# Kernel optimization log

Measured on AMD Instinct MI355X. Metric: run time of the kernel, lower is better.

Reference implementation:

```python
import jax, jax.numpy as jnp
import numpy as np

D_IN = 1024
D_OUT = 1024
B = 4
S = 2048


def setup_inputs() -> dict:
    key = jax.random.key(0)
    kx, kq, kk, kv = jax.random.split(key, 4)
    x = jax.random.normal(kx, (B, S, D_IN), dtype=jnp.float32)
    # Linear weights stored as [d_in, d_out] so projection is x @ W
    sc = 1.0 / np.sqrt(D_IN)
    Wq = jax.random.normal(kq, (D_IN, D_OUT), dtype=jnp.float32) * sc
    Wk = jax.random.normal(kk, (D_IN, D_OUT), dtype=jnp.float32) * sc
    Wv = jax.random.normal(kv, (D_IN, D_OUT), dtype=jnp.float32) * sc
    return {"x": x, "Wq": Wq, "Wk": Wk, "Wv": Wv}


def reference(x, Wq, Wk, Wv):
    # q, k, v: [b, s, d_out]
    q = jnp.einsum("bsd,de->bse", x, Wq)
    k = jnp.einsum("bsd,de->bse", x, Wk)
    v = jnp.einsum("bsd,de->bse", x, Wv)
    s = q.shape[1]
    # raw scores [b, s, s]
    scores = jnp.einsum("bqd,bkd->bqk", q, k)
    # causal mask: disallow key j > query i (see notes re: original mask bug)
    causal = jnp.triu(jnp.ones((s, s), dtype=bool), k=1)
    scores = jnp.where(causal[None, :, :], -jnp.inf, scores)
    scale = 1.0 / jnp.sqrt(jnp.asarray(k.shape[-1], dtype=scores.dtype))
    att_weights = jax.nn.softmax(scores * scale, axis=-1)
    # dropout p=0.0 -> identity
    att_output = jnp.einsum("bqk,bkd->bqd", att_weights, v)
    return att_output, att_weights
```

## Files before the change

### kernel.cpp

```cpp
#include <hip/hip_runtime.h>
#include <stdint.h>

#define DIM 1024
#define SEQ 2048
#define NB 4

typedef unsigned short u16;
typedef __bf16 bf16x8 __attribute__((ext_vector_type(8)));
typedef float floatx4 __attribute__((ext_vector_type(4)));

__device__ __forceinline__ u16 f32_to_bf16(float f) {
  union { float f; unsigned u; } v; v.f = f;
  unsigned r = v.u + 0x7FFFu + ((v.u >> 16) & 1u);
  return (u16)(r >> 16);
}

__device__ __forceinline__ void async16(const void* g, void* l) {
  __builtin_amdgcn_global_load_lds(
      (__attribute__((address_space(1))) unsigned int*)g,
      (__attribute__((address_space(3))) unsigned int*)l, 16, 0, 0);
}

__global__ __launch_bounds__(256) void k_prep(const float* __restrict__ x,
                                              const float* __restrict__ Wq,
                                              const float* __restrict__ Wk,
                                              const float* __restrict__ Wv,
                                              u16* __restrict__ xb,
                                              u16* __restrict__ wt) {
  __shared__ u16 tile[32][33];
  const int bid = blockIdx.x;
  const int tid = threadIdx.x;
  if (bid < 8192) {
    int i = bid * 256 + tid;
    float4 v = ((const float4*)x)[i];
    ushort4 o;
    o.x = f32_to_bf16(v.x); o.y = f32_to_bf16(v.y);
    o.z = f32_to_bf16(v.z); o.w = f32_to_bf16(v.w);
    ((ushort4*)xb)[i] = o;
  } else {
    int t = bid - 8192;
    int z = t >> 10;
    int ti = t & 1023;
    int c0 = (ti & 31) * 32, r0 = (ti >> 5) * 32;
    const float* src = (z == 0) ? Wq : (z == 1) ? Wk : Wv;
    u16* d = wt + (size_t)z * DIM * DIM;
    int tx = tid & 31, ty = tid >> 5;
    #pragma unroll
    for (int dy = 0; dy < 32; dy += 8)
      tile[ty + dy][tx] = f32_to_bf16(src[(size_t)(r0 + ty + dy) * DIM + c0 + tx]);
    __syncthreads();
    #pragma unroll
    for (int dy = 0; dy < 32; dy += 8)
      d[(size_t)(c0 + ty + dy) * DIM + r0 + tx] = tile[tx][ty + dy];
  }
}

__device__ __forceinline__ void mfma_core(const u16* __restrict__ A, int lda,
                                          const u16* __restrict__ Bt, int ldb,
                                          int ktiles, u16* lds,
                                          floatx4 acc[4][4]) {
  const int tid = threadIdx.x;
  const int lane = tid & 63;
  const int wid = tid >> 6;
  u16* lds_a = lds;
  u16* lds_b = lds + 8192;

  const int srow = lane >> 3;
  const int sg = (lane & 7) ^ (srow & 7);
  const u16* ag = A + (size_t)(wid * 32 + srow) * lda + sg * 8;
  const u16* bg = Bt + (size_t)(wid * 32 + srow) * ldb + sg * 8;
  u16* la = lds_a + wid * 2048;
  u16* lb = lds_b + wid * 2048;

  const int wm = (wid >> 1) * 64, wn = (wid & 1) * 64;
  const int lrow = lane & 15, quad = lane >> 4;
  const int s = lrow & 7;
  const int g0 = (quad ^ s) * 8;
  const int g1 = ((quad + 4) ^ s) * 8;
  const u16* pa = lds_a + (wm + lrow) * 64;
  const u16* pb = lds_b + (wn + lrow) * 64;

  for (int kt = 0; kt < ktiles; ++kt) {
    #pragma unroll
    for (int c = 0; c < 4; ++c) {
      async16(ag + (size_t)c * 8 * lda, la + c * 512);
      async16(bg + (size_t)c * 8 * ldb, lb + c * 512);
    }
    ag += 64; bg += 64;
    __syncthreads();
    #pragma unroll
    for (int ks = 0; ks < 2; ++ks) {
      const int g = ks ? g1 : g0;
      bf16x8 af[4], bfr[4];
      #pragma unroll
      for (int t = 0; t < 4; ++t) af[t] = *(const bf16x8*)(pa + t * 1024 + g);
      #pragma unroll
      for (int t = 0; t < 4; ++t) bfr[t] = *(const bf16x8*)(pb + t * 1024 + g);
      #pragma unroll
      for (int i = 0; i < 4; ++i)
        #pragma unroll
        for (int j = 0; j < 4; ++j)
          acc[i][j] = __builtin_amdgcn_mfma_f32_16x16x32_bf16(af[i], bfr[j],
                                                              acc[i][j], 0, 0, 0);
    }
    __syncthreads();
  }
}

__global__ __launch_bounds__(256) void k_proj(const u16* __restrict__ xb,
                                              const u16* __restrict__ wt,
                                              u16* __restrict__ qk,
                                              u16* __restrict__ vT) {
  const int id = blockIdx.x;
  const int z2 = id >> 9;
  const int r = id & 511;
  const int g = (r >> 6) * 8 + (r & 7);
  const int h = (r >> 3) & 7;
  __shared__ u16 lds[16384];
  floatx4 acc[4][4] = {};
  const u16 *A, *Bt;
  if (z2 < 2) {
    A = xb + (size_t)g * 128 * DIM;
    Bt = wt + (size_t)z2 * DIM * DIM + (size_t)h * 128 * DIM;
  } else {
    A = wt + (size_t)2 * DIM * DIM + (size_t)h * 128 * DIM;
    Bt = xb + (size_t)g * 128 * DIM;
  }
  mfma_core(A, DIM, Bt, DIM, DIM / 64, lds, acc);
  const int lane = threadIdx.x & 63, wid = threadIdx.x >> 6;
  const int wm = (wid >> 1) * 64, wn = (wid & 1) * 64;
  const int lrow = lane & 15, quad = lane >> 4;
  if (z2 < 2) {
    u16* C = qk + (size_t)z2 * (NB * SEQ * DIM)
                + (size_t)(g * 128 + wm + quad * 4) * DIM + h * 128 + wn + lrow;
    #pragma unroll
    for (int i = 0; i < 4; ++i)
      #pragma unroll
      for (int rr = 0; rr < 4; ++rr)
        #pragma unroll
        for (int j = 0; j < 4; ++j)
          C[(size_t)(i * 16 + rr) * DIM + j * 16] = f32_to_bf16(acc[i][j][rr]);
  } else {
    const int t0 = g * 128;
    const int b = t0 >> 11, s0 = t0 & 2047;
    u16* C = vT + (size_t)b * (DIM * SEQ)
                + (size_t)(h * 128 + wm + quad * 4) * SEQ + s0 + wn + lrow;
    #pragma unroll
    for (int i = 0; i < 4; ++i)
      #pragma unroll
      for (int rr = 0; rr < 4; ++rr)
        #pragma unroll
        for (int j = 0; j < 4; ++j)
          C[(size_t)(i * 16 + rr) * SEQ + j * 16] = f32_to_bf16(acc[i][j][rr]);
  }
}

__global__ __launch_bounds__(256) void k_scores(const u16* __restrict__ q,
                                                const u16* __restrict__ k,
                                                float* __restrict__ w) {
  const int id = blockIdx.x;
  const int b = id & 3;
  int t = id >> 2;
  int mt = (int)((sqrtf(8.0f * (float)t + 1.0f) - 1.0f) * 0.5f);
  while ((mt + 1) * (mt + 2) / 2 <= t) ++mt;
  while (mt * (mt + 1) / 2 > t) --mt;
  const int nt = t - mt * (mt + 1) / 2;
  __shared__ u16 lds[16384];
  floatx4 acc[4][4] = {};
  mfma_core(q + (size_t)b * SEQ * DIM + (size_t)mt * 128 * DIM, DIM,
            k + (size_t)b * SEQ * DIM + (size_t)nt * 128 * DIM, DIM,
            DIM / 64, lds, acc);
  const int lane = threadIdx.x & 63, wid = threadIdx.x >> 6;
  const int wm = (wid >> 1) * 64, wn = (wid & 1) * 64;
  const int lrow = lane & 15, quad = lane >> 4;
  float* C = w + (size_t)b * SEQ * SEQ
               + (size_t)(mt * 128 + wm + quad * 4) * SEQ + nt * 128 + wn + lrow;
  #pragma unroll
  for (int i = 0; i < 4; ++i)
    #pragma unroll
    for (int rr = 0; rr < 4; ++rr)
      #pragma unroll
      for (int j = 0; j < 4; ++j)
        C[(size_t)(i * 16 + rr) * SEQ + j * 16] = acc[i][j][rr] * 0.03125f;
}

__global__ __launch_bounds__(256) void k_softmax(float* __restrict__ w,
                                                 u16* __restrict__ P) {
  const int r = blockIdx.x;
  const int i = r & (SEQ - 1);
  const int len = i + 1;
  const int plen4 = (((i >> 7) + 1) << 7) >> 2;
  float4* srow = (float4*)(w + (size_t)r * SEQ);
  ushort4* prow = (ushort4*)(P + (size_t)r * SEQ);
  const int tid = threadIdx.x;
  const int lane = tid & 63, wid = tid >> 6;
  __shared__ float rm[4], rs[4];

  float4 e[2];
  float mx = -1e30f;
  #pragma unroll
  for (int u = 0; u < 2; ++u) {
    int q4 = tid + u * 256;
    int j0 = q4 * 4;
    float4 v = make_float4(-1e30f, -1e30f, -1e30f, -1e30f);
    if (j0 < len) {
      v = srow[q4];
      v.x = (j0 + 0 < len) ? v.x : -1e30f;
      v.y = (j0 + 1 < len) ? v.y : -1e30f;
      v.z = (j0 + 2 < len) ? v.z : -1e30f;
      v.w = (j0 + 3 < len) ? v.w : -1e30f;
    }
    e[u] = v;
    mx = fmaxf(mx, fmaxf(fmaxf(v.x, v.y), fmaxf(v.z, v.w)));
  }
  #pragma unroll
  for (int o = 32; o >= 1; o >>= 1) mx = fmaxf(mx, __shfl_xor(mx, o, 64));
  if (lane == 0) rm[wid] = mx;
  __syncthreads();
  mx = fmaxf(fmaxf(rm[0], rm[1]), fmaxf(rm[2], rm[3]));

  float sum = 0.f;
  #pragma unroll
  for (int u = 0; u < 2; ++u) {
    e[u].x = __expf(e[u].x - mx);
    e[u].y = __expf(e[u].y - mx);
    e[u].z = __expf(e[u].z - mx);
    e[u].w = __expf(e[u].w - mx);
    sum += e[u].x + e[u].y + e[u].z + e[u].w;
  }
  #pragma unroll
  for (int o = 32; o >= 1; o >>= 1) sum += __shfl_xor(sum, o, 64);
  if (lane == 0) rs[wid] = sum;
  __syncthreads();
  sum = rs[0] + rs[1] + rs[2] + rs[3];
  const float inv = 1.0f / sum;

  #pragma unroll
  for (int u = 0; u < 2; ++u) {
    int q4 = tid + u * 256;
    int j0 = q4 * 4;
    float4 v;
    v.x = (j0 + 0 < len) ? e[u].x * inv : 0.f;
    v.y = (j0 + 1 < len) ? e[u].y * inv : 0.f;
    v.z = (j0 + 2 < len) ? e[u].z * inv : 0.f;
    v.w = (j0 + 3 < len) ? e[u].w * inv : 0.f;
    srow[q4] = v;
    if (q4 < plen4) {
      ushort4 p;
      p.x = f32_to_bf16(v.x); p.y = f32_to_bf16(v.y);
      p.z = f32_to_bf16(v.z); p.w = f32_to_bf16(v.w);
      prow[q4] = p;
    }
  }
}

__global__ __launch_bounds__(256) void k_pv(const u16* __restrict__ P,
                                            const u16* __restrict__ vT,
                                            float* __restrict__ out) {
  const int id = blockIdx.x;
  const int mt = 15 - (id >> 5);
  const int nt = (id >> 2) & 7;
  const int b = id & 3;
  __shared__ u16 lds[16384];
  floatx4 acc[4][4] = {};
  mfma_core(P + (size_t)b * SEQ * SEQ + (size_t)mt * 128 * SEQ, SEQ,
            vT + (size_t)b * DIM * SEQ + (size_t)nt * 128 * SEQ, SEQ,
            2 * (mt + 1), lds, acc);
  const int lane = threadIdx.x & 63, wid = threadIdx.x >> 6;
  const int wm = (wid >> 1) * 64, wn = (wid & 1) * 64;
  const int lrow = lane & 15, quad = lane >> 4;
  float* C = out + (size_t)b * SEQ * DIM
                 + (size_t)(mt * 128 + wm + quad * 4) * DIM + nt * 128 + wn + lrow;
  #pragma unroll
  for (int i = 0; i < 4; ++i)
    #pragma unroll
    for (int rr = 0; rr < 4; ++rr)
      #pragma unroll
      for (int j = 0; j < 4; ++j)
        C[(size_t)(i * 16 + rr) * DIM + j * 16] = acc[i][j][rr];
}

extern "C" void kernel_launch(void* const* d_in, const int* in_sizes, int n_in,
                              void* d_out, int out_size, void* d_ws, size_t ws_size,
                              hipStream_t stream) {
  const float* x  = (const float*)d_in[0];
  const float* Wq = (const float*)d_in[1];
  const float* Wk = (const float*)d_in[2];
  const float* Wv = (const float*)d_in[3];
  float* att_out = (float*)d_out;
  float* att_w   = (float*)d_out + 8388608;

  u16* xb = (u16*)d_ws;
  u16* wt = xb + 8388608;
  u16* qk = wt + 3145728;
  u16* vT = qk + 16777216;
  u16* P  = vT + 8388608;

  k_prep<<<11264, 256, 0, stream>>>(x, Wq, Wk, Wv, xb, wt);
  k_proj<<<1536, 256, 0, stream>>>(xb, wt, qk, vT);
  k_scores<<<544, 256, 0, stream>>>(qk, qk + 8388608, att_w);
  k_softmax<<<8192, 256, 0, stream>>>(att_w, P);
  k_pv<<<512, 256, 0, stream>>>(P, vT, att_out);
}
```

Before: 276.1 us.

## Use 128-wide K tiles with XOR-swizzled LDS in scores and PV GEMMs

Adds an mfma_core128 variant that stages 128-deep K slices of A and B into LDS with an XOR swizzle, halving the number of barrier-separated k-iterations in k_scores and k_pv. It is meant to cut synchronization overhead per MFMA and reduce LDS bank conflicts, at the cost of doubling shared memory per block, which may lower occupancy. Separately, the x-to-bf16 conversion in k_prep now handles two float4 per thread with half as many blocks.

```diff
diff --git a/kernel.cpp b/kernel.cpp
--- a/kernel.cpp
+++ b/kernel.cpp
@@ -30,15 +30,19 @@
   __shared__ u16 tile[32][33];
   const int bid = blockIdx.x;
   const int tid = threadIdx.x;
-  if (bid < 8192) {
+  if (bid < 4096) {
     int i = bid * 256 + tid;
-    float4 v = ((const float4*)x)[i];
-    ushort4 o;
-    o.x = f32_to_bf16(v.x); o.y = f32_to_bf16(v.y);
-    o.z = f32_to_bf16(v.z); o.w = f32_to_bf16(v.w);
-    ((ushort4*)xb)[i] = o;
+    float4 a = ((const float4*)x)[i * 2];
+    float4 b = ((const float4*)x)[i * 2 + 1];
+    ushort4 o0, o1;
+    o0.x = f32_to_bf16(a.x); o0.y = f32_to_bf16(a.y);
+    o0.z = f32_to_bf16(a.z); o0.w = f32_to_bf16(a.w);
+    o1.x = f32_to_bf16(b.x); o1.y = f32_to_bf16(b.y);
+    o1.z = f32_to_bf16(b.z); o1.w = f32_to_bf16(b.w);
+    ((ushort4*)xb)[i * 2] = o0;
+    ((ushort4*)xb)[i * 2 + 1] = o1;
   } else {
-    int t = bid - 8192;
+    int t = bid - 4096;
     int z = t >> 10;
     int ti = t & 1023;
     int c0 = (ti & 31) * 32, r0 = (ti >> 5) * 32;
@@ -96,6 +100,64 @@
       for (int t = 0; t < 4; ++t) af[t] = *(const bf16x8*)(pa + t * 1024 + g);
       #pragma unroll
       for (int t = 0; t < 4; ++t) bfr[t] = *(const bf16x8*)(pb + t * 1024 + g);
+      #pragma unroll
+      for (int i = 0; i < 4; ++i)
+        #pragma unroll
+        for (int j = 0; j < 4; ++j)
+          acc[i][j] = __builtin_amdgcn_mfma_f32_16x16x32_bf16(af[i], bfr[j],
+                                                              acc[i][j], 0, 0, 0);
+    }
+    __syncthreads();
+  }
+}
+
+__device__ __forceinline__ void mfma_core128(const u16* __restrict__ A, int lda,
+                                             const u16* __restrict__ Bt, int ldb,
+                                             int kchunks, u16* lds,
+                                             floatx4 acc[4][4]) {
+  const int tid = threadIdx.x;
+  const int lane = tid & 63;
+  const int wid = tid >> 6;
+  u16* lds_a = lds;
+  u16* lds_b = lds + 16384;
+
+  const int srow4 = lane >> 4;
+  const int sgr = lane & 15;
+  const int gbase = sgr ^ srow4;
+  const u16* ag0 = A + (size_t)(wid * 32 + srow4) * lda + gbase * 8;
+  const u16* ag1 = A + (size_t)(wid * 32 + srow4) * lda + (gbase ^ 4) * 8;
+  const u16* bg0 = Bt + (size_t)(wid * 32 + srow4) * ldb + gbase * 8;
+  const u16* bg1 = Bt + (size_t)(wid * 32 + srow4) * ldb + (gbase ^ 4) * 8;
+  u16* la = lds_a + wid * 4096;
+  u16* lb = lds_b + wid * 4096;
+
+  const int wm = (wid >> 1) * 64, wn = (wid & 1) * 64;
+  const int lrow = lane & 15, quad = lane >> 4;
+  const int s = lrow & 7;
+  const u16* pa = lds_a + (wm + lrow) * 128;
+  const u16* pb = lds_b + (wn + lrow) * 128;
+
+  for (int kt = 0; kt < kchunks; ++kt) {
+    #pragma unroll
+    for (int c = 0; c < 8; ++c) {
+      const u16* sa = ((c & 1) ? ag1 : ag0) + (size_t)(c * 4) * lda;
+      async16(sa, la + c * 512);
+    }
+    #pragma unroll
+    for (int c = 0; c < 8; ++c) {
+      const u16* sb = ((c & 1) ? bg1 : bg0) + (size_t)(c * 4) * ldb;
+      async16(sb, lb + c * 512);
+    }
+    ag0 += 128; ag1 += 128; bg0 += 128; bg1 += 128;
+    __syncthreads();
+    #pragma unroll
+    for (int ks = 0; ks < 4; ++ks) {
+      const int g = (((ks << 2) | quad) ^ s) << 3;
+      bf16x8 af[4], bfr[4];
+      #pragma unroll
+      for (int t = 0; t < 4; ++t) af[t] = *(const bf16x8*)(pa + t * 2048 + g);
+      #pragma unroll
+      for (int t = 0; t < 4; ++t) bfr[t] = *(const bf16x8*)(pb + t * 2048 + g);
       #pragma unroll
       for (int i = 0; i < 4; ++i)
         #pragma unroll
@@ -165,11 +227,11 @@
   while ((mt + 1) * (mt + 2) / 2 <= t) ++mt;
   while (mt * (mt + 1) / 2 > t) --mt;
   const int nt = t - mt * (mt + 1) / 2;
-  __shared__ u16 lds[16384];
+  __shared__ u16 lds[32768];
   floatx4 acc[4][4] = {};
-  mfma_core(q + (size_t)b * SEQ * DIM + (size_t)mt * 128 * DIM, DIM,
-            k + (size_t)b * SEQ * DIM + (size_t)nt * 128 * DIM, DIM,
-            DIM / 64, lds, acc);
+  mfma_core128(q + (size_t)b * SEQ * DIM + (size_t)mt * 128 * DIM, DIM,
+               k + (size_t)b * SEQ * DIM + (size_t)nt * 128 * DIM, DIM,
+               DIM / 128, lds, acc);
   const int lane = threadIdx.x & 63, wid = threadIdx.x >> 6;
   const int wm = (wid >> 1) * 64, wn = (wid & 1) * 64;
   const int lrow = lane & 15, quad = lane >> 4;
@@ -261,11 +323,11 @@
   const int mt = 15 - (id >> 5);
   const int nt = (id >> 2) & 7;
   const int b = id & 3;
-  __shared__ u16 lds[16384];
+  __shared__ u16 lds[32768];
   floatx4 acc[4][4] = {};
-  mfma_core(P + (size_t)b * SEQ * SEQ + (size_t)mt * 128 * SEQ, SEQ,
-            vT + (size_t)b * DIM * SEQ + (size_t)nt * 128 * SEQ, SEQ,
-            2 * (mt + 1), lds, acc);
+  mfma_core128(P + (size_t)b * SEQ * SEQ + (size_t)mt * 128 * SEQ, SEQ,
+               vT + (size_t)b * DIM * SEQ + (size_t)nt * 128 * SEQ, SEQ,
+               mt + 1, lds, acc);
   const int lane = threadIdx.x & 63, wid = threadIdx.x >> 6;
   const int wm = (wid >> 1) * 64, wn = (wid & 1) * 64;
   const int lrow = lane & 15, quad = lane >> 4;
@@ -296,7 +358,7 @@
   u16* vT = qk + 16777216;
   u16* P  = vT + 8388608;
 
-  k_prep<<<11264, 256, 0, stream>>>(x, Wq, Wk, Wv, xb, wt);
+  k_prep<<<7168, 256, 0, stream>>>(x, Wq, Wk, Wv, xb, wt);
   k_proj<<<1536, 256, 0, stream>>>(xb, wt, qk, vT);
   k_scores<<<544, 256, 0, stream>>>(qk, qk + 8388608, att_w);
   k_softmax<<<8192, 256, 0, stream>>>(att_w, P);
```

Measured after the change: 273.7 us. Within noise of the previous version (-0.9%).
